# Performance work log

Hardware: AMD Instinct MI355X
Metric: run time of the kernel (lower is better)

## Reference

```python
import jax, jax.numpy as jnp
import numpy as np

NUM_STEPS = 100  # constructor default


def setup_inputs() -> dict:
    key = jax.random.key(0)
    x = jax.random.uniform(key, (2048, 1024), dtype=jnp.float32)  # [batch, features] in [0,1]
    return {"x": x}


def reference(x) -> jnp.ndarray:
    """Latency-encoding branch of TemporalSpikeCoder.encode, vectorized.

    Torch original: spike_times = ((1 - x) * num_steps).long(); then a Python
    double loop writes spike_train[b, t, f] = 1.0 when t < num_steps.
    Here that is a single masked one-hot comparison along the time axis.
    """
    spike_times = ((1.0 - x) * NUM_STEPS).astype(jnp.int32)        # [B, F]
    t = jnp.arange(NUM_STEPS, dtype=jnp.int32)                      # [T]
    # one-hot over time; entries with spike_times == NUM_STEPS (x == 0)
    # match no t in [0, NUM_STEPS) and therefore stay zero, exactly like
    # the `if t < num_steps` guard in the original.
    spike_train = (spike_times[:, None, :] == t[None, :, None]).astype(jnp.float32)  # [B, T, F]
    return spike_train
```

## Files before the change

kernel.cpp:

```cpp
#include <hip/hip_runtime.h>
#include <hip/hip_bf16.h>


constexpr int F  = 1024;
constexpr int T  = 100;
constexpr int F4 = F / 4;

typedef float v4f __attribute__((ext_vector_type(4)));

__global__ __launch_bounds__(256) void TemporalSpikeCoder_78125455114738_kernel(
    const float* __restrict__ x, float* __restrict__ out, int total4) {
    const int gsz = gridDim.x * blockDim.x;
    const v4f* __restrict__ x4 = reinterpret_cast<const v4f*>(x);
    v4f* __restrict__ o4 = reinterpret_cast<v4f*>(out);

    for (int i = blockIdx.x * blockDim.x + threadIdx.x; i < total4; i += gsz) {
        const unsigned f4 = (unsigned)i & (F4 - 1);
        const unsigned bt = (unsigned)i >> 8;
        const unsigned b  = bt / T;
        const int      t  = (int)(bt - b * T);

        const v4f xv = x4[b * F4 + f4];
        v4f v;
        v.x = ((int)((1.0f - xv.x) * 100.0f) == t) ? 1.0f : 0.0f;
        v.y = ((int)((1.0f - xv.y) * 100.0f) == t) ? 1.0f : 0.0f;
        v.z = ((int)((1.0f - xv.z) * 100.0f) == t) ? 1.0f : 0.0f;
        v.w = ((int)((1.0f - xv.w) * 100.0f) == t) ? 1.0f : 0.0f;

        o4[i] = v;
    }
}

extern "C" void kernel_launch(void* const* d_in, const int* in_sizes, int n_in,
                              void* d_out, int out_size, void* d_ws, size_t ws_size,
                              hipStream_t stream) {
    const float* x = (const float*)d_in[0];
    float* out = (float*)d_out;
    const int total4 = out_size / 4;
    const int block = 256;
    const int grid = 2048;
    TemporalSpikeCoder_78125455114738_kernel<<<grid, block, 0, stream>>>(x, out, total4);
}
```

Measured before the change: 873.4 us.

## Compute spike times once per row and stream timesteps per thread

Each block now owns 8 batch rows. Each thread loads its x vector once per row, converts it to a spike time in registers, then loops over all timesteps writing one-hot vectors. This removes the per-element division/modulo index math and the repeated x reloads of the grid-stride loop. In exchange the grid shrinks to one block per 8 rows, so fewer waves are resident and store parallelism relies on per-thread unrolling.

```diff
diff --git a/kernel.cpp b/kernel.cpp
--- a/kernel.cpp
+++ b/kernel.cpp
@@ -2,32 +2,42 @@
 #include <hip/hip_bf16.h>
 
 
-constexpr int F  = 1024;
-constexpr int T  = 100;
-constexpr int F4 = F / 4;
+constexpr int F   = 1024;
+constexpr int T   = 100;
+constexpr int F4  = F / 4;
+constexpr int RPB = 8;
 
 typedef float v4f __attribute__((ext_vector_type(4)));
 
 __global__ __launch_bounds__(256) void TemporalSpikeCoder_78125455114738_kernel(
-    const float* __restrict__ x, float* __restrict__ out, int total4) {
-    const int gsz = gridDim.x * blockDim.x;
+    const float* __restrict__ x, float* __restrict__ out) {
+    const int b0 = blockIdx.x * RPB;
+    const int f4 = threadIdx.x;
+
     const v4f* __restrict__ x4 = reinterpret_cast<const v4f*>(x);
     v4f* __restrict__ o4 = reinterpret_cast<v4f*>(out);
 
-    for (int i = blockIdx.x * blockDim.x + threadIdx.x; i < total4; i += gsz) {
-        const unsigned f4 = (unsigned)i & (F4 - 1);
-        const unsigned bt = (unsigned)i >> 8;
-        const unsigned b  = bt / T;
-        const int      t  = (int)(bt - b * T);
+    int sx[RPB], sy[RPB], sz[RPB], sw[RPB];
+    #pragma unroll
+    for (int r = 0; r < RPB; ++r) {
+        const v4f xv = x4[(b0 + r) * F4 + f4];
+        sx[r] = (int)((1.0f - xv.x) * 100.0f);
+        sy[r] = (int)((1.0f - xv.y) * 100.0f);
+        sz[r] = (int)((1.0f - xv.z) * 100.0f);
+        sw[r] = (int)((1.0f - xv.w) * 100.0f);
+    }
 
-        const v4f xv = x4[b * F4 + f4];
-        v4f v;
-        v.x = ((int)((1.0f - xv.x) * 100.0f) == t) ? 1.0f : 0.0f;
-        v.y = ((int)((1.0f - xv.y) * 100.0f) == t) ? 1.0f : 0.0f;
-        v.z = ((int)((1.0f - xv.z) * 100.0f) == t) ? 1.0f : 0.0f;
-        v.w = ((int)((1.0f - xv.w) * 100.0f) == t) ? 1.0f : 0.0f;
-
-        o4[i] = v;
+    v4f* o = o4 + (size_t)b0 * (T * F4) + f4;
+    for (int t = 0; t < T; ++t) {
+        #pragma unroll
+        for (int r = 0; r < RPB; ++r) {
+            v4f v;
+            v.x = (sx[r] == t) ? 1.0f : 0.0f;
+            v.y = (sy[r] == t) ? 1.0f : 0.0f;
+            v.z = (sz[r] == t) ? 1.0f : 0.0f;
+            v.w = (sw[r] == t) ? 1.0f : 0.0f;
+            o[(size_t)r * (T * F4) + (size_t)t * F4] = v;
+        }
     }
 }
 
@@ -36,8 +46,7 @@
                               hipStream_t stream) {
     const float* x = (const float*)d_in[0];
     float* out = (float*)d_out;
-    const int total4 = out_size / 4;
-    const int block = 256;
-    const int grid = 2048;
-    TemporalSpikeCoder_78125455114738_kernel<<<grid, block, 0, stream>>>(x, out, total4);
+    const int B = in_sizes[0] / F;
+    const int grid = B / RPB;
+    TemporalSpikeCoder_78125455114738_kernel<<<grid, 256, 0, stream>>>(x, out);
 }
```

New measurement: 814.2 us. -6.8%, faster.
